# Kernel tuning notes

Hardware: AMD Instinct MI355X
Metric: run time of the kernel (lower is better)

## Reference

```python
import jax, jax.numpy as jnp
import numpy as np

SEQ, EMB, OUT = 8192, 1024, 128

def setup_inputs() -> dict:
    key = jax.random.key(0)
    k1, k2, k3, k4 = jax.random.split(key, 4)
    return {
        "x": jax.random.normal(k1, (SEQ, EMB), dtype=jnp.float32),
        "wquery": jax.random.normal(k2, (EMB, OUT), dtype=jnp.float32) * (2.0 / EMB) ** 0.5,
        "wkey": jax.random.normal(k3, (EMB, OUT), dtype=jnp.float32) * (2.0 / EMB) ** 0.5,
        "wvalue": jax.random.normal(k4, (EMB, OUT), dtype=jnp.float32) * (2.0 / EMB) ** 0.5,
    }

def reference(x, wquery, wkey, wvalue):
    # Single-head attention, mask=True branch (mask tensor is zeros -> no masking).
    q = x @ wquery   # [S, D]
    k = x @ wkey     # [S, D]
    v = x @ wvalue   # [S, D]
    scale = jnp.sqrt(jnp.asarray(q.shape[-1], dtype=q.dtype))
    a = (q @ k.T) / scale              # [S, S]
    p = jax.nn.softmax(a, axis=1)      # softmax over keys (dim=1 in torch)
    return p @ v                       # [S, D]
```

## Files before the change

kernel.cpp:

```cpp
#include <hip/hip_runtime.h>
#include <cstdint>
#include <cstddef>

#define SEQ 8192
#define EMB 1024
#define DH  128

typedef __bf16 bf16x8 __attribute__((ext_vector_type(8)));
typedef __bf16 bf16x2 __attribute__((ext_vector_type(2)));
typedef float  f32x4  __attribute__((ext_vector_type(4)));
typedef float  f32x16 __attribute__((ext_vector_type(16)));
typedef uint32_t u32x4 __attribute__((ext_vector_type(4)));
typedef unsigned short u16x8 __attribute__((ext_vector_type(8)));

static constexpr float QSCALE = (float)(1.4426950408889634 / 11.313708498984760);

__device__ __forceinline__ unsigned short f2bf(float f) {
  uint32_t u = __builtin_bit_cast(uint32_t, f);
  u += 0x7FFFu + ((u >> 16) & 1u);
  return (unsigned short)(u >> 16);
}
__device__ __forceinline__ float bf2f(unsigned short u) {
  return __builtin_bit_cast(float, (uint32_t)u << 16);
}

#define GLD_LDS16(gsrc, ldst) \
  __builtin_amdgcn_global_load_lds((__attribute__((address_space(1))) void*)(gsrc), \
                                   (__attribute__((address_space(3))) void*)(ldst), 16, 0, 0)

__global__ __launch_bounds__(256) void convert_kernel(
    const float* __restrict__ x,
    const float* __restrict__ wq, const float* __restrict__ wk, const float* __restrict__ wv,
    unsigned short* __restrict__ xb, unsigned short* __restrict__ wt)
{
  const int bid = blockIdx.x;
  const int t = threadIdx.x;
  if (bid < 2048) {
    size_t e = (size_t)bid * 4096 + (size_t)t * 16;
#pragma unroll
    for (int i = 0; i < 2; ++i) {
      float4 a = *reinterpret_cast<const float4*>(x + e + i * 8);
      float4 b = *reinterpret_cast<const float4*>(x + e + i * 8 + 4);
      u16x8 o = { f2bf(a.x), f2bf(a.y), f2bf(a.z), f2bf(a.w),
                  f2bf(b.x), f2bf(b.y), f2bf(b.z), f2bf(b.w) };
      *reinterpret_cast<u16x8*>(xb + e + i * 8) = o;
    }
  } else {
    const int which = (bid - 2048) >> 2;
    const int k = ((bid - 2048) & 3) * 256 + t;
    const float* w = (which == 0) ? wq : ((which == 1) ? wk : wv);
    const float scl = (which == 0) ? QSCALE : 1.0f;
#pragma unroll
    for (int n = 0; n < 128; n += 4) {
      float4 v = *reinterpret_cast<const float4*>(w + (size_t)k * DH + n);
      wt[((size_t)which * DH + n + 0) * EMB + k] = f2bf(v.x * scl);
      wt[((size_t)which * DH + n + 1) * EMB + k] = f2bf(v.y * scl);
      wt[((size_t)which * DH + n + 2) * EMB + k] = f2bf(v.z * scl);
      wt[((size_t)which * DH + n + 3) * EMB + k] = f2bf(v.w * scl);
    }
  }
}

__global__ __launch_bounds__(256) void qkv_gemm(
    const unsigned short* __restrict__ xb, const unsigned short* __restrict__ wt,
    unsigned short* __restrict__ qs, unsigned short* __restrict__ ks,
    unsigned short* __restrict__ vt)
{
  __shared__ char LDS[49152];
  char* A0 = LDS;
  char* B0 = LDS + 16384;
  unsigned short* T = (unsigned short*)LDS;

  const int t    = threadIdx.x;
  const int lane = t & 63;
  const int wid  = t >> 6;
  const int wr   = wid >> 1, wc = wid & 1;
  const int l31  = lane & 31;
  const int hi   = lane >> 5;
  const int row0 = blockIdx.x * 64;
  const int which = blockIdx.y;

  const char* xc  = (const char*)xb;
  const char* wtc = (const char*)(wt + (size_t)which * DH * EMB);

  f32x16 acc[2] = {};

  auto STAGE = [&](int buf, int k0) {
#pragma unroll
    for (int i = 0; i < 2; ++i) {
      int bidx = i * 4096 + t * 16;
      int row = bidx >> 7, off = bidx & 127;
      const char* src = xc + (size_t)(row0 + row) * (EMB * 2) + k0 * 2 + (off ^ ((row & 7) << 4));
      GLD_LDS16(src, A0 + buf * 8192 + i * 4096 + wid * 1024);
    }
#pragma unroll
    for (int i = 0; i < 4; ++i) {
      int bidx = i * 4096 + t * 16;
      int n = bidx >> 7, off = bidx & 127;
      const char* src = wtc + (size_t)n * (EMB * 2) + k0 * 2 + (off ^ ((n & 7) << 4));
      GLD_LDS16(src, B0 + buf * 16384 + i * 4096 + wid * 1024);
    }
  };

  STAGE(0, 0);
  int cur = 0;
  for (int it = 0; it < EMB / 64; ++it) {
    if (it + 1 < EMB / 64) {
      STAGE(cur ^ 1, (it + 1) * 64);
      asm volatile("s_waitcnt vmcnt(6)" ::: "memory");
    } else {
      asm volatile("s_waitcnt vmcnt(0)" ::: "memory");
    }
    __builtin_amdgcn_s_barrier();
    asm volatile("" ::: "memory");

    const char* Ab = A0 + cur * 8192;
    const char* Bb = B0 + cur * 16384;
    const int ar   = wr * 32 + l31;
    const int aswz = (l31 & 7) << 4;

    __builtin_amdgcn_s_setprio(1);
#pragma unroll
    for (int kk = 0; kk < 4; ++kk) {
      bf16x8 af = *reinterpret_cast<const bf16x8*>(Ab + ar * 128 + ((kk * 32 + hi * 16) ^ aswz));
#pragma unroll
      for (int nt = 0; nt < 2; ++nt) {
        const int n = wc * 64 + nt * 32 + l31;
        bf16x8 bf = *reinterpret_cast<const bf16x8*>(Bb + n * 128 + ((kk * 32 + hi * 16) ^ ((n & 7) << 4)));
        acc[nt] = __builtin_amdgcn_mfma_f32_32x32x16_bf16(af, bf, acc[nt], 0, 0, 0);
      }
    }
    __builtin_amdgcn_s_setprio(0);

    asm volatile("" ::: "memory");
    __builtin_amdgcn_s_barrier();
    asm volatile("" ::: "memory");
    cur ^= 1;
  }

  if (which < 2) {
    unsigned short* dst = (which == 0) ? qs : ks;
#pragma unroll
    for (int nt = 0; nt < 2; ++nt)
#pragma unroll
      for (int r = 0; r < 16; ++r) {
        int row = row0 + wr * 32 + (r & 3) + 8 * (r >> 2) + 4 * hi;
        dst[(size_t)row * DH + wc * 64 + nt * 32 + l31] = f2bf(acc[nt][r]);
      }
  } else {
    __syncthreads();
#pragma unroll
    for (int nt = 0; nt < 2; ++nt)
#pragma unroll
      for (int r = 0; r < 16; ++r) {
        int d  = wc * 64 + nt * 32 + l31;
        int rl = wr * 32 + (r & 3) + 8 * (r >> 2) + 4 * hi;
        T[d * 72 + rl] = f2bf(acc[nt][r]);
      }
    __syncthreads();
    const int d = t >> 1, half = t & 1;
#pragma unroll
    for (int i = 0; i < 4; ++i) {
      uint4 v = *reinterpret_cast<const uint4*>(&T[d * 72 + half * 32 + i * 8]);
      *reinterpret_cast<uint4*>(vt + (size_t)d * SEQ + row0 + half * 32 + i * 8) = v;
    }
  }
}

template <int NS>
__global__ __launch_bounds__(512, 2) void attn_kernel(
    const unsigned short* __restrict__ qs, const unsigned short* __restrict__ ks,
    const unsigned short* __restrict__ vt,
    unsigned short* __restrict__ Obf, float* __restrict__ ml)
{
  __shared__ unsigned short Ks[2][64 * 128];
  __shared__ unsigned short Vt[2][128 * 64];

  const int t    = threadIdx.x;
  const int lane = t & 63;
  const int wid  = t >> 6;
  const int l31  = lane & 31;
  const int hi   = lane >> 5;
  const int swz  = (lane & 7) << 4;
  const int q0   = blockIdx.x * 256 + wid * 32;
  const int sp   = blockIdx.y;

  bf16x8 qf[8];
  {
    const unsigned short* qp = qs + (size_t)(q0 + l31) * DH + hi * 8;
#pragma unroll
    for (int ds = 0; ds < 8; ++ds)
      qf[ds] = *reinterpret_cast<const bf16x8*>(qp + ds * 16);
  }

  float m = -__builtin_inff();
  float l = 0.f;
  f32x16 O[4] = {};

  const char* ksc = (const char*)ks;
  const char* vtc = (const char*)vt;
  char* ksl = (char*)&Ks[0][0];
  char* vtl = (char*)&Vt[0][0];

  constexpr int CHUNK = SEQ / NS;
  constexpr int NT = CHUNK / 64;
  const int kv_base = sp * CHUNK;

  auto STAGE = [&](int buf, int it) {
    const int kv0 = kv_base + it * 64;
#pragma unroll
    for (int rr = 0; rr < 2; ++rr) {
      int bidx = rr * 512 + t;
      int key = bidx >> 4, blk = bidx & 15;
      const char* src = ksc + (size_t)(kv0 + key) * 256 + ((blk * 16) ^ ((key & 7) << 4));
      GLD_LDS16(src, ksl + buf * 16384 + rr * 8192 + wid * 1024);
    }
#pragma unroll
    for (int rr = 0; rr < 2; ++rr) {
      int bidx = rr * 512 + t;
      int d = bidx >> 3, kb = bidx & 7;
      const char* src = vtc + (size_t)d * (SEQ * 2) + (size_t)kv0 * 2 + ((kb * 16) ^ ((d & 7) << 4));
      GLD_LDS16(src, vtl + buf * 16384 + rr * 8192 + wid * 1024);
    }
  };

  auto build2 = [&](const f32x16& P, bf16x8* fr) {
    uint32_t c[8];
#pragma unroll
    for (int i = 0; i < 8; ++i) {
      bf16x2 b2; b2[0] = (__bf16)P[2 * i]; b2[1] = (__bf16)P[2 * i + 1];
      c[i] = __builtin_bit_cast(uint32_t, b2);
    }
    uint32_t r0 = __shfl_xor(c[0], 32, 64), r1 = __shfl_xor(c[1], 32, 64);
    uint32_t r2 = __shfl_xor(c[2], 32, 64), r3 = __shfl_xor(c[3], 32, 64);
    u32x4 w0;
    w0[0] = hi ? r2 : c[0];
    w0[1] = hi ? r3 : c[1];
    w0[2] = hi ? c[2] : r0;
    w0[3] = hi ? c[3] : r1;
    uint32_t r4 = __shfl_xor(c[4], 32, 64), r5 = __shfl_xor(c[5], 32, 64);
    uint32_t r6 = __shfl_xor(c[6], 32, 64), r7 = __shfl_xor(c[7], 32, 64);
    u32x4 w1;
    w1[0] = hi ? r6 : c[4];
    w1[1] = hi ? r7 : c[5];
    w1[2] = hi ? c[6] : r4;
    w1[3] = hi ? c[7] : r5;
    fr[0] = __builtin_bit_cast(bf16x8, w0);
    fr[1] = __builtin_bit_cast(bf16x8, w1);
  };

  STAGE(0, 0);

  int cur = 0;
  for (int it = 0; it < NT; ++it) {
    asm volatile("s_waitcnt vmcnt(0)" ::: "memory");
    __builtin_amdgcn_s_barrier();
    asm volatile("" ::: "memory");

    if (it + 1 < NT) STAGE(cur ^ 1, it + 1);

    const char* kbase = ksl + cur * 16384;
    const char* vbase = vtl + cur * 16384;

    f32x16 S0 = {}, S1 = {};
    __builtin_amdgcn_s_setprio(1);
#pragma unroll
    for (int ds = 0; ds < 8; ++ds) {
      bf16x8 ka = *reinterpret_cast<const bf16x8*>(kbase + l31 * 256 + ((ds * 32 + hi * 16) ^ swz));
      S0 = __builtin_amdgcn_mfma_f32_32x32x16_bf16(ka, qf[ds], S0, 0, 0, 0);
    }
#pragma unroll
    for (int ds = 0; ds < 8; ++ds) {
      bf16x8 ka = *reinterpret_cast<const bf16x8*>(kbase + 8192 + l31 * 256 + ((ds * 32 + hi * 16) ^ swz));
      S1 = __builtin_amdgcn_mfma_f32_32x32x16_bf16(ka, qf[ds], S1, 0, 0, 0);
    }
    __builtin_amdgcn_s_setprio(0);

    float mx[16];
#pragma unroll
    for (int r = 0; r < 16; ++r) mx[r] = fmaxf(S0[r], S1[r]);
#pragma unroll
    for (int st = 8; st >= 1; st >>= 1)
#pragma unroll
      for (int r = 0; r < st; ++r) mx[r] = fmaxf(mx[r], mx[r + st]);
    const float pm = fmaxf(mx[0], __shfl_xor(mx[0], 32, 64));

    if (__any(pm > m + 11.0f)) {
      float mn = fmaxf(m, pm);
      float corr = __builtin_amdgcn_exp2f(m - mn);
      m = mn;
      l *= corr;
#pragma unroll
      for (int r = 0; r < 16; ++r) {
        float cr = __shfl(corr, (r & 3) + 8 * (r >> 2) + 4 * hi, 64);
#pragma unroll
        for (int nt = 0; nt < 4; ++nt) O[nt][r] *= cr;
      }
    }
    float sm[16];
#pragma unroll
    for (int r = 0; r < 16; ++r) {
      S0[r] = __builtin_amdgcn_exp2f(S0[r] - m);
      S1[r] = __builtin_amdgcn_exp2f(S1[r] - m);
      sm[r] = S0[r] + S1[r];
    }
#pragma unroll
    for (int st = 8; st >= 1; st >>= 1)
#pragma unroll
      for (int r = 0; r < st; ++r) sm[r] += sm[r + st];
    l += sm[0] + __shfl_xor(sm[0], 32, 64);

    bf16x8 pa[4];
    build2(S0, &pa[0]);
    build2(S1, &pa[2]);

    __builtin_amdgcn_s_setprio(1);
#pragma unroll
    for (int ks4 = 0; ks4 < 4; ++ks4) {
#pragma unroll
      for (int nt = 0; nt < 4; ++nt) {
        const int d = nt * 32 + l31;
        bf16x8 vb = *reinterpret_cast<const bf16x8*>(vbase + d * 128 + ((ks4 * 32 + hi * 16) ^ swz));
        O[nt] = __builtin_amdgcn_mfma_f32_32x32x16_bf16(pa[ks4], vb, O[nt], 0, 0, 0);
      }
    }
    __builtin_amdgcn_s_setprio(0);

    cur ^= 1;
  }

  const float linv = 1.0f / l;
  unsigned short* Obase = Obf + ((size_t)sp * SEQ + q0) * DH;
#pragma unroll
  for (int r = 0; r < 16; ++r) {
    const int row = (r & 3) + 8 * (r >> 2) + 4 * hi;
    const float li = __shfl(linv, row, 64);
#pragma unroll
    for (int nt = 0; nt < 4; ++nt)
      Obase[(size_t)row * DH + nt * 32 + l31] = f2bf(O[nt][r] * li);
  }
  if (lane < 32) {
    ml[(size_t)sp * (2 * SEQ) + q0 + lane]       = m;
    ml[(size_t)sp * (2 * SEQ) + SEQ + q0 + lane] = l;
  }
}

template <int NS>
__global__ __launch_bounds__(256) void combine_kernel(
    const unsigned short* __restrict__ Obf, const float* __restrict__ ml, float* __restrict__ out)
{
  const int idx = blockIdx.x * 256 + threadIdx.x;
  const int s = idx >> 4;
  const int c = (idx & 15) * 8;
  float mv[NS], lv[NS];
  float M = -__builtin_inff();
#pragma unroll
  for (int i = 0; i < NS; ++i) {
    mv[i] = ml[(size_t)i * (2 * SEQ) + s];
    lv[i] = ml[(size_t)i * (2 * SEQ) + SEQ + s];
    M = fmaxf(M, mv[i]);
  }
  float den = 0.f;
  float num[8] = {};
#pragma unroll
  for (int i = 0; i < NS; ++i) {
    float g = __builtin_amdgcn_exp2f(mv[i] - M) * lv[i];
    den += g;
    u16x8 o = *reinterpret_cast<const u16x8*>(&Obf[((size_t)i * SEQ + s) * DH + c]);
#pragma unroll
    for (int j = 0; j < 8; ++j) num[j] += g * bf2f(o[j]);
  }
  const float inv = 1.f / den;
  f32x4 r0, r1;
#pragma unroll
  for (int j = 0; j < 4; ++j) { r0[j] = num[j] * inv; r1[j] = num[j + 4] * inv; }
  *reinterpret_cast<f32x4*>(&out[(size_t)s * DH + c])     = r0;
  *reinterpret_cast<f32x4*>(&out[(size_t)s * DH + c + 4]) = r1;
}

extern "C" void kernel_launch(void* const* d_in, const int* in_sizes, int n_in,
                              void* d_out, int out_size, void* d_ws, size_t ws_size,
                              hipStream_t stream) {
  const float* x  = (const float*)d_in[0];
  const float* wq = (const float*)d_in[1];
  const float* wk = (const float*)d_in[2];
  const float* wv = (const float*)d_in[3];
  float* out = (float*)d_out;

  char* ws = (char*)d_ws;
  const size_t MB = 1024 * 1024;
  unsigned short* qs = (unsigned short*)(ws);
  unsigned short* ks = (unsigned short*)(ws + 2 * MB);
  unsigned short* vt = (unsigned short*)(ws + 4 * MB);
  unsigned short* wt = (unsigned short*)(ws + 6 * MB);
  unsigned short* xb = (unsigned short*)(ws + 6 * MB + 768 * 1024);

  convert_kernel<<<2048 + 12, 256, 0, stream>>>(x, wq, wk, wv, xb, wt);
  qkv_gemm<<<dim3(SEQ / 64, 3), 256, 0, stream>>>(xb, wt, qs, ks, vt);

  unsigned short* Obf = (unsigned short*)(ws + 6 * MB);
  const size_t need8 = 6 * MB + 8ull * SEQ * DH * 2 + 8ull * 2 * SEQ * 4;
  if (ws_size >= need8) {
    float* ml = (float*)(ws + 6 * MB + 8ull * SEQ * DH * 2);
    attn_kernel<8><<<dim3(SEQ / 256, 8), 512, 0, stream>>>(qs, ks, vt, Obf, ml);
    combine_kernel<8><<<SEQ * DH / 8 / 256, 256, 0, stream>>>(Obf, ml, out);
  } else {
    float* ml = (float*)(ws + 6 * MB + 4ull * SEQ * DH * 2);
    attn_kernel<4><<<dim3(SEQ / 256, 4), 512, 0, stream>>>(qs, ks, vt, Obf, ml);
    combine_kernel<4><<<SEQ * DH / 8 / 256, 256, 0, stream>>>(Obf, ml, out);
  }
}
```

Before: 85.54 us.

## Software-pipeline QK^T one tile ahead of softmax and PV in attention loop

Restructures the flash-attention main loop so that the QK^T MFMAs for tile it+1 are issued before the softmax and PV of tile it. K is prefetched two tiles ahead and V one tile ahead, in separate staging lambdas, and the loop is unrolled by two to ping-pong the score registers. The goal is to overlap matrix-core work with the exp/reduction VALU work and hide global-to-LDS latency. It costs an extra 32 live accumulator registers, which may lower occupancy, and it assumes NT is even. The LDS buffer indexing by tile parity must stay race-free across the barrier placement.

```diff
diff --git a/kernel.cpp b/kernel.cpp
--- a/kernel.cpp
+++ b/kernel.cpp
@@ -206,21 +206,40 @@
   constexpr int NT = CHUNK / 64;
   const int kv_base = sp * CHUNK;
 
-  auto STAGE = [&](int buf, int it) {
-    const int kv0 = kv_base + it * 64;
+  auto KSTAGE = [&](int tile) {
+    const int kv0 = kv_base + tile * 64;
 #pragma unroll
     for (int rr = 0; rr < 2; ++rr) {
       int bidx = rr * 512 + t;
       int key = bidx >> 4, blk = bidx & 15;
       const char* src = ksc + (size_t)(kv0 + key) * 256 + ((blk * 16) ^ ((key & 7) << 4));
-      GLD_LDS16(src, ksl + buf * 16384 + rr * 8192 + wid * 1024);
-    }
+      GLD_LDS16(src, ksl + (tile & 1) * 16384 + rr * 8192 + wid * 1024);
+    }
+  };
+  auto VSTAGE = [&](int tile) {
+    const int kv0 = kv_base + tile * 64;
 #pragma unroll
     for (int rr = 0; rr < 2; ++rr) {
       int bidx = rr * 512 + t;
       int d = bidx >> 3, kb = bidx & 7;
       const char* src = vtc + (size_t)d * (SEQ * 2) + (size_t)kv0 * 2 + ((kb * 16) ^ ((d & 7) << 4));
-      GLD_LDS16(src, vtl + buf * 16384 + rr * 8192 + wid * 1024);
+      GLD_LDS16(src, vtl + (tile & 1) * 16384 + rr * 8192 + wid * 1024);
+    }
+  };
+
+  auto QKT = [&](f32x16& T0, f32x16& T1, int tile) {
+    const char* kb = ksl + (tile & 1) * 16384;
+    f32x16 z = {};
+    T0 = z; T1 = z;
+#pragma unroll
+    for (int ds = 0; ds < 8; ++ds) {
+      bf16x8 ka = *reinterpret_cast<const bf16x8*>(kb + l31 * 256 + ((ds * 32 + hi * 16) ^ swz));
+      T0 = __builtin_amdgcn_mfma_f32_32x32x16_bf16(ka, qf[ds], T0, 0, 0, 0);
+    }
+#pragma unroll
+    for (int ds = 0; ds < 8; ++ds) {
+      bf16x8 ka = *reinterpret_cast<const bf16x8*>(kb + 8192 + l31 * 256 + ((ds * 32 + hi * 16) ^ swz));
+      T1 = __builtin_amdgcn_mfma_f32_32x32x16_bf16(ka, qf[ds], T1, 0, 0, 0);
     }
   };
 
@@ -249,36 +268,19 @@
     fr[1] = __builtin_bit_cast(bf16x8, w1);
   };
 
-  STAGE(0, 0);
-
-  int cur = 0;
-  for (int it = 0; it < NT; ++it) {
-    asm volatile("s_waitcnt vmcnt(0)" ::: "memory");
-    __builtin_amdgcn_s_barrier();
-    asm volatile("" ::: "memory");
-
-    if (it + 1 < NT) STAGE(cur ^ 1, it + 1);
-
-    const char* kbase = ksl + cur * 16384;
-    const char* vbase = vtl + cur * 16384;
-
-    f32x16 S0 = {}, S1 = {};
-    __builtin_amdgcn_s_setprio(1);
-#pragma unroll
-    for (int ds = 0; ds < 8; ++ds) {
-      bf16x8 ka = *reinterpret_cast<const bf16x8*>(kbase + l31 * 256 + ((ds * 32 + hi * 16) ^ swz));
-      S0 = __builtin_amdgcn_mfma_f32_32x32x16_bf16(ka, qf[ds], S0, 0, 0, 0);
-    }
-#pragma unroll
-    for (int ds = 0; ds < 8; ++ds) {
-      bf16x8 ka = *reinterpret_cast<const bf16x8*>(kbase + 8192 + l31 * 256 + ((ds * 32 + hi * 16) ^ swz));
-      S1 = __builtin_amdgcn_mfma_f32_32x32x16_bf16(ka, qf[ds], S1, 0, 0, 0);
-    }
-    __builtin_amdgcn_s_setprio(0);
+  auto BODY = [&](int it, f32x16& Sc0, f32x16& Sc1, f32x16& Sn0, f32x16& Sn1) {
+    if (it + 2 < NT) KSTAGE(it + 2);
+    if (it + 1 < NT) VSTAGE(it + 1);
+
+    if (it + 1 < NT) {
+      __builtin_amdgcn_s_setprio(1);
+      QKT(Sn0, Sn1, it + 1);
+      __builtin_amdgcn_s_setprio(0);
+    }
 
     float mx[16];
 #pragma unroll
-    for (int r = 0; r < 16; ++r) mx[r] = fmaxf(S0[r], S1[r]);
+    for (int r = 0; r < 16; ++r) mx[r] = fmaxf(Sc0[r], Sc1[r]);
 #pragma unroll
     for (int st = 8; st >= 1; st >>= 1)
 #pragma unroll
@@ -300,9 +302,9 @@
     float sm[16];
 #pragma unroll
     for (int r = 0; r < 16; ++r) {
-      S0[r] = __builtin_amdgcn_exp2f(S0[r] - m);
-      S1[r] = __builtin_amdgcn_exp2f(S1[r] - m);
-      sm[r] = S0[r] + S1[r];
+      Sc0[r] = __builtin_amdgcn_exp2f(Sc0[r] - m);
+      Sc1[r] = __builtin_amdgcn_exp2f(Sc1[r] - m);
+      sm[r] = Sc0[r] + Sc1[r];
     }
 #pragma unroll
     for (int st = 8; st >= 1; st >>= 1)
@@ -311,22 +313,41 @@
     l += sm[0] + __shfl_xor(sm[0], 32, 64);
 
     bf16x8 pa[4];
-    build2(S0, &pa[0]);
-    build2(S1, &pa[2]);
-
+    build2(Sc0, &pa[0]);
+    build2(Sc1, &pa[2]);
+
+    const char* vb0 = vtl + (it & 1) * 16384;
     __builtin_amdgcn_s_setprio(1);
 #pragma unroll
     for (int ks4 = 0; ks4 < 4; ++ks4) {
 #pragma unroll
       for (int nt = 0; nt < 4; ++nt) {
         const int d = nt * 32 + l31;
-        bf16x8 vb = *reinterpret_cast<const bf16x8*>(vbase + d * 128 + ((ks4 * 32 + hi * 16) ^ swz));
+        bf16x8 vb = *reinterpret_cast<const bf16x8*>(vb0 + d * 128 + ((ks4 * 32 + hi * 16) ^ swz));
         O[nt] = __builtin_amdgcn_mfma_f32_32x32x16_bf16(pa[ks4], vb, O[nt], 0, 0, 0);
       }
     }
     __builtin_amdgcn_s_setprio(0);
 
-    cur ^= 1;
+    asm volatile("s_waitcnt vmcnt(0)" ::: "memory");
+    __builtin_amdgcn_s_barrier();
+    asm volatile("" ::: "memory");
+  };
+
+  KSTAGE(0); VSTAGE(0); KSTAGE(1);
+  asm volatile("s_waitcnt vmcnt(0)" ::: "memory");
+  __builtin_amdgcn_s_barrier();
+  asm volatile("" ::: "memory");
+
+  f32x16 Sa0, Sa1, Sb0, Sb1;
+  QKT(Sa0, Sa1, 0);
+  asm volatile("" ::: "memory");
+  __builtin_amdgcn_s_barrier();
+  asm volatile("" ::: "memory");
+
+  for (int it = 0; it < NT; it += 2) {
+    BODY(it,     Sa0, Sa1, Sb0, Sb1);
+    BODY(it + 1, Sb0, Sb1, Sa0, Sa1);
   }
 
   const float linv = 1.0f / l;
```

Result: no change. 83.93 us (-1.9%).
